# Kernel optimization log

Hardware: AMD Instinct MI355X
Metric: run time of the kernel (lower is better)

The kernel has to match this reference:

```python
import jax, jax.numpy as jnp
import numpy as np

B, N_L, N_T, H, NG, E, M = 8, 64, 512, 128, 10, 2048, 4096
BN_EPS = 1e-5


def _bn(x, g, b, m, v):
    # eval-mode BatchNorm1d
    return (x - m) * jax.lax.rsqrt(v + BN_EPS) * g + b


def _to_dense_batch(x, batch, n_batch, n_max):
    # batch is sorted; position within each graph = idx - first idx of that graph
    first = jnp.searchsorted(batch, jnp.arange(n_batch))
    pos = jnp.arange(x.shape[0]) - first[batch]
    dense = jnp.zeros((n_batch, n_max, x.shape[-1]), x.dtype).at[batch, pos].set(x)
    mask = jnp.zeros((n_batch, n_max), bool).at[batch, pos].set(True)
    return dense, mask


def setup_inputs() -> dict:
    key = jax.random.key(0)
    ks = jax.random.split(key, 32)
    rn = lambda k, s, sc=0.05: (jax.random.normal(k, s, jnp.float32) * sc)
    inp = {}
    inp["lig_s"] = rn(ks[0], (B * N_L, H), 1.0)
    inp["pro_s"] = rn(ks[1], (B * N_T, H), 1.0)
    inp["lig_batch"] = jnp.repeat(jnp.arange(B), N_L)
    inp["pro_batch"] = jnp.repeat(jnp.arange(B), N_T)
    inp["donar_idx"] = jax.random.randint(ks[2], (M,), 0, B * N_L * N_T, jnp.int32)
    inp["edge_index"] = jax.random.randint(ks[3], (2, E), 0, B * N_L, jnp.int32)
    # MLP head (Linear 2H->H + BN)
    inp["mlp_w"] = rn(ks[4], (2 * H, H)); inp["mlp_b"] = rn(ks[5], (H,))
    inp["mlp_g"] = 1.0 + rn(ks[6], (H,), 0.1); inp["mlp_be"] = rn(ks[7], (H,))
    inp["mlp_m"] = rn(ks[8], (H,)); inp["mlp_v"] = jax.random.uniform(ks[9], (H,), jnp.float32) + 0.5
    # start_donar_selector (Linear 2H->H + BN + Linear H->1 + sigmoid)
    inp["sel_w1"] = rn(ks[10], (2 * H, H)); inp["sel_b1"] = rn(ks[11], (H,))
    inp["sel_g"] = 1.0 + rn(ks[12], (H,), 0.1); inp["sel_be"] = rn(ks[13], (H,))
    inp["sel_m"] = rn(ks[14], (H,)); inp["sel_v"] = jax.random.uniform(ks[15], (H,), jnp.float32) + 0.5
    inp["sel_w2"] = rn(ks[16], (H, 1)); inp["sel_b2"] = rn(ks[17], (1,))
    # MDN heads
    inp["pi_w"] = rn(ks[18], (H, NG)); inp["pi_b"] = rn(ks[19], (NG,))
    inp["sg_w"] = rn(ks[20], (H, NG)); inp["sg_b"] = rn(ks[21], (NG,))
    inp["mu_w"] = rn(ks[22], (H, NG)); inp["mu_b"] = rn(ks[23], (NG,))
    # atom / bond type heads
    inp["at_w"] = rn(ks[24], (H, 18)); inp["at_b"] = rn(ks[25], (18,))
    inp["bt_w"] = rn(ks[26], (2 * H, 5)); inp["bt_b"] = rn(ks[27], (5,))
    return inp


def reference(lig_s, pro_s, lig_batch, pro_batch, donar_idx, edge_index,
              mlp_w, mlp_b, mlp_g, mlp_be, mlp_m, mlp_v,
              sel_w1, sel_b1, sel_g, sel_be, sel_m, sel_v, sel_w2, sel_b2,
              pi_w, pi_b, sg_w, sg_b, mu_w, mu_b, at_w, at_b, bt_w, bt_b):
    h_l, l_mask = _to_dense_batch(lig_s, lig_batch, B, N_L)   # (B,N_L,H)
    h_t, t_mask = _to_dense_batch(pro_s, pro_batch, B, N_T)   # (B,N_T,H)
    # dense pairwise broadcast + concat (masks are all-True by construction,
    # so C[C_mask] == flatten)
    pl = jnp.broadcast_to(h_l[:, :, None, :], (B, N_L, N_T, H))
    pt = jnp.broadcast_to(h_t[:, None, :, :], (B, N_L, N_T, H))
    Cpair = jnp.concatenate([pl, pt], -1).reshape(B * N_L * N_T, 2 * H)
    C_mask = l_mask[:, :, None] & t_mask[:, None, :]
    # donor-metal selector on gathered pairs
    dm = Cpair[donar_idx]
    sel_h = jax.nn.elu(_bn(dm @ sel_w1 + sel_b1, sel_g, sel_be, sel_m, sel_v))
    coordinated_donar = jax.nn.sigmoid(sel_h @ sel_w2 + sel_b2)[:, 0]
    # shared pair MLP (dropout is identity in eval)
    Ch = jax.nn.elu(_bn(Cpair @ mlp_w + mlp_b, mlp_g, mlp_be, mlp_m, mlp_v))
    pi = jax.nn.softmax(Ch @ pi_w + pi_b, -1)
    sigma = jax.nn.elu(Ch @ sg_w + sg_b) + 1.1
    mu = jax.nn.elu(Ch @ mu_w + mu_b) + 1.0
    C_batch = jnp.repeat(jnp.arange(B), N_L * N_T)
    atom_types = lig_s @ at_w + at_b
    bond_types = jnp.concatenate([lig_s[edge_index[0]], lig_s[edge_index[1]]], 1) @ bt_w + bt_b
    return (pi, sigma, mu, C_batch, atom_types, bond_types, coordinated_donar, C_mask)
```

## Files before the change

kernel.cpp:

```cpp
#include <hip/hip_runtime.h>

#define NL 64
#define NT 512
#define BB 8
#define HH 128
#define NE 2048
#define NM 4096

static constexpr size_t OUT_PI = 0;
static constexpr size_t OUT_SG = 2621440;
static constexpr size_t OUT_MU = 5242880;
static constexpr size_t OUT_CB = 7864320;
static constexpr size_t OUT_AT = 8126464;
static constexpr size_t OUT_BT = 8135680;
static constexpr size_t OUT_CD = 8145920;
static constexpr size_t OUT_CM = 8150016;

__device__ __forceinline__ float bf2f(ushort u) {
    union { uint i; float f; } v; v.i = ((uint)u) << 16; return v.f;
}
__device__ __forceinline__ float bflo(uint u) {
    union { uint i; float f; } v; v.i = u << 16; return v.f;
}
__device__ __forceinline__ float bfhi(uint u) {
    union { uint i; float f; } v; v.i = u & 0xffff0000u; return v.f;
}
__device__ __forceinline__ ushort f2bf(float f) {
    union { float f; uint u; } v; v.f = f;
    uint u = v.u + 0x7fffu + ((v.u >> 16) & 1u);
    return (ushort)(u >> 16);
}
__device__ __forceinline__ float eluf(float x) { return x > 0.f ? x : (__expf(x) - 1.f); }

__device__ __forceinline__ float ldv(const float* p, int i) { return p[i]; }
__device__ __forceinline__ float ldv(const ushort* p, int i) { return bf2f(p[i]); }

template <typename T>
__device__ void prep_w_body(const T* piw, const T* pib, const T* sgw, const T* sgb,
                            const T* muw, const T* mub, const T* selw2, const T* selb2,
                            float* Wp, float* biasv, float* sel2f) {
    int k = threadIdx.x;
#pragma unroll
    for (int g = 0; g < 10; ++g) {
        Wp[k * 32 + g]      = ldv(piw, k * 10 + g);
        Wp[k * 32 + 10 + g] = ldv(sgw, k * 10 + g);
        Wp[k * 32 + 20 + g] = ldv(muw, k * 10 + g);
    }
    Wp[k * 32 + 30] = 0.f; Wp[k * 32 + 31] = 0.f;
    sel2f[k] = ldv(selw2, k);
    if (k == 0) {
#pragma unroll
        for (int g = 0; g < 10; ++g) {
            biasv[g] = ldv(pib, g); biasv[10 + g] = ldv(sgb, g); biasv[20 + g] = ldv(mub, g);
        }
        biasv[30] = 0.f; biasv[31] = 0.f;
        sel2f[128] = ldv(selb2, 0);
    }
}
__global__ void kprep0(const uint* sniffsrc, const void* piw, const void* pib,
                       const void* sgw, const void* sgb, const void* muw, const void* mub,
                       const void* selw2, const void* selb2,
                       int* flag, float* Wp, float* biasv, float* sel2f) {
    __shared__ int sflag;
    if (threadIdx.x == 0) {
        int c = 0;
        for (int i = 0; i < 32; ++i) {
            uint lo = sniffsrc[i] & 0xFFFFu;
            if (lo >= 0x3F00u && lo <= 0x3FC0u) ++c;
        }
        sflag = (c >= 24) ? 0 : 1;
        *flag = sflag;
    }
    __syncthreads();
    if (sflag) prep_w_body((const float*)piw, (const float*)pib, (const float*)sgw, (const float*)sgb,
                           (const float*)muw, (const float*)mub, (const float*)selw2, (const float*)selb2,
                           Wp, biasv, sel2f);
    else       prep_w_body((const ushort*)piw, (const ushort*)pib, (const ushort*)sgw, (const ushort*)sgb,
                           (const ushort*)muw, (const ushort*)mub, (const ushort*)selw2, (const ushort*)selb2,
                           Wp, biasv, sel2f);
}

template <typename T>
__device__ void prep_lig_body(const T* lig, const T* mlpw, const T* selw1,
                              const T* mg, const T* mv, const T* sg_, const T* sv,
                              const T* atw, const T* atb,
                              float* Lp, float* SLp, float* out) {
    __shared__ float x[HH];
    int r = blockIdx.x, n = threadIdx.x;
    x[n] = ldv(lig, r * HH + n);
    __syncthreads();
    float accL = 0.f, accS = 0.f;
#pragma unroll 8
    for (int k = 0; k < HH; ++k) {
        float xv = x[k];
        accL = fmaf(xv, ldv(mlpw, k * HH + n), accL);
        accS = fmaf(xv, ldv(selw1, k * HH + n), accS);
    }
    float sM = ldv(mg, n) * rsqrtf(ldv(mv, n) + 1e-5f);
    float sS = ldv(sg_, n) * rsqrtf(ldv(sv, n) + 1e-5f);
    Lp[r * HH + n]  = accL * sM;
    SLp[r * HH + n] = accS * sS;
    if (n < 18) {
        float a = 0.f;
#pragma unroll 8
        for (int k = 0; k < HH; ++k) a = fmaf(x[k], ldv(atw, k * 18 + n), a);
        out[OUT_AT + r * 18 + n] = a + ldv(atb, n);
    }
}
__global__ void kprep_lig(const void* lig, const void* mlpw, const void* selw1,
                          const void* mg, const void* mv, const void* sg_, const void* sv,
                          const void* atw, const void* atb, const int* flag,
                          float* Lp, float* SLp, float* out) {
    if (*flag) prep_lig_body((const float*)lig, (const float*)mlpw, (const float*)selw1,
                             (const float*)mg, (const float*)mv, (const float*)sg_, (const float*)sv,
                             (const float*)atw, (const float*)atb, Lp, SLp, out);
    else       prep_lig_body((const ushort*)lig, (const ushort*)mlpw, (const ushort*)selw1,
                             (const ushort*)mg, (const ushort*)mv, (const ushort*)sg_, (const ushort*)sv,
                             (const ushort*)atw, (const ushort*)atb, Lp, SLp, out);
}

template <typename T>
__device__ void prep_pro_bond_body(const T* pro, const T* mlpw, const T* selw1,
                                   const T* mb, const T* mg, const T* mbe, const T* mm, const T* mv,
                                   const T* sb1, const T* sg_, const T* sbe, const T* sm, const T* sv,
                                   const T* lig, const int* edge, const T* btw, const T* btb,
                                   ushort* Tp, ushort* STp, float* out) {
    __shared__ float x[4][HH];
    int r0 = blockIdx.x * 4, n = threadIdx.x;
#pragma unroll
    for (int r = 0; r < 4; ++r) x[r][n] = ldv(pro, (r0 + r) * HH + n);
    __syncthreads();
    float aT0 = 0, aT1 = 0, aT2 = 0, aT3 = 0, aS0 = 0, aS1 = 0, aS2 = 0, aS3 = 0;
#pragma unroll 4
    for (int k = 0; k < HH; ++k) {
        float wM = ldv(mlpw, (HH + k) * HH + n);
        float wS = ldv(selw1, (HH + k) * HH + n);
        float x0 = x[0][k], x1 = x[1][k], x2 = x[2][k], x3 = x[3][k];
        aT0 = fmaf(x0, wM, aT0); aS0 = fmaf(x0, wS, aS0);
        aT1 = fmaf(x1, wM, aT1); aS1 = fmaf(x1, wS, aS1);
        aT2 = fmaf(x2, wM, aT2); aS2 = fmaf(x2, wS, aS2);
        aT3 = fmaf(x3, wM, aT3); aS3 = fmaf(x3, wS, aS3);
    }
    float sM = ldv(mg, n) * rsqrtf(ldv(mv, n) + 1e-5f);
    float sS = ldv(sg_, n) * rsqrtf(ldv(sv, n) + 1e-5f);
    float offM = ldv(mb, n) * sM + ldv(mbe, n) - ldv(mm, n) * sM;
    float offS = ldv(sb1, n) * sS + ldv(sbe, n) - ldv(sm, n) * sS;
    Tp[(r0 + 0) * HH + n] = f2bf(aT0 * sM + offM);  STp[(r0 + 0) * HH + n] = f2bf(aS0 * sS + offS);
    Tp[(r0 + 1) * HH + n] = f2bf(aT1 * sM + offM);  STp[(r0 + 1) * HH + n] = f2bf(aS1 * sS + offS);
    Tp[(r0 + 2) * HH + n] = f2bf(aT2 * sM + offM);  STp[(r0 + 2) * HH + n] = f2bf(aS2 * sS + offS);
    Tp[(r0 + 3) * HH + n] = f2bf(aT3 * sM + offM);  STp[(r0 + 3) * HH + n] = f2bf(aS3 * sS + offS);

    int widx = n >> 6, lane = n & 63;
    int e = blockIdx.x * 2 + widx;
    int e0 = edge[e], e1 = edge[NE + e];
    int k0 = lane * 2;
    float a0 = ldv(lig, e0 * HH + k0), a1 = ldv(lig, e0 * HH + k0 + 1);
    float b0 = ldv(lig, e1 * HH + k0), b1 = ldv(lig, e1 * HH + k0 + 1);
    float acc[5];
#pragma unroll
    for (int c = 0; c < 5; ++c) {
        acc[c] = a0 * ldv(btw, k0 * 5 + c) + a1 * ldv(btw, (k0 + 1) * 5 + c)
               + b0 * ldv(btw, (HH + k0) * 5 + c) + b1 * ldv(btw, (HH + k0 + 1) * 5 + c);
    }
#pragma unroll
    for (int c = 0; c < 5; ++c)
        for (int off = 32; off > 0; off >>= 1) acc[c] += __shfl_xor(acc[c], off, 64);
    if (lane == 0) {
#pragma unroll
        for (int c = 0; c < 5; ++c) out[OUT_BT + e * 5 + c] = acc[c] + ldv(btb, c);
    }
}
__global__ void kprep_pro_bond(const void* pro, const void* mlpw, const void* selw1,
                               const void* mb, const void* mg, const void* mbe, const void* mm, const void* mv,
                               const void* sb1, const void* sg_, const void* sbe, const void* sm, const void* sv,
                               const void* lig, const int* edge, const void* btw, const void* btb,
                               const int* flag, ushort* Tp, ushort* STp, float* out) {
    if (*flag) prep_pro_bond_body((const float*)pro, (const float*)mlpw, (const float*)selw1,
                                  (const float*)mb, (const float*)mg, (const float*)mbe, (const float*)mm, (const float*)mv,
                                  (const float*)sb1, (const float*)sg_, (const float*)sbe, (const float*)sm, (const float*)sv,
                                  (const float*)lig, edge, (const float*)btw, (const float*)btb, Tp, STp, out);
    else       prep_pro_bond_body((const ushort*)pro, (const ushort*)mlpw, (const ushort*)selw1,
                                  (const ushort*)mb, (const ushort*)mg, (const ushort*)mbe, (const ushort*)mm, (const ushort*)mv,
                                  (const ushort*)sb1, (const ushort*)sg_, (const ushort*)sbe, (const ushort*)sm, (const ushort*)sv,
                                  (const ushort*)lig, edge, (const ushort*)btw, (const ushort*)btb, Tp, STp, out);
}

__global__ __launch_bounds__(256, 4) void kmain(const ushort* __restrict__ Tp, const float* __restrict__ Lp,
                                                const float* __restrict__ Wp, const float* __restrict__ biasv,
                                                const float* __restrict__ SLp, const ushort* __restrict__ STp,
                                                const int* __restrict__ donar, const float* __restrict__ sel2f,
                                                float* __restrict__ out) {
    __shared__ uint  ldsTu[64 * 65];
    __shared__ float ldsL[4 * 132];
    int bid = blockIdx.x;
    int jt = bid & 7, it = (bid >> 3) & 15, b = bid >> 7;
    int j0 = jt * 64, i0 = it * 4;
    int tid = threadIdx.x;

    const uint* srcT = (const uint*)(Tp + (size_t)(b * NT + j0) * HH);
#pragma unroll
    for (int q = 0; q < 4; ++q) {
        int t = tid + q * 256;
        uint4 v = ((const uint4*)srcT)[t];
        int j = t >> 4, c0 = (t & 15) * 4;
        uint* dst = &ldsTu[j * 65 + c0];
        dst[0] = v.x; dst[1] = v.y; dst[2] = v.z; dst[3] = v.w;
    }
    if (tid < 128) {
        int r = tid >> 5, c = (tid & 31) * 4;
        float4 v = *(const float4*)(Lp + (size_t)(b * NL + i0 + r) * HH + c);
        *(float4*)&ldsL[r * 132 + c] = v;
    }
    __syncthreads();

    int lane_j = tid & 63, widx = tid >> 6;
    const uint*  trowp = &ldsTu[lane_j * 65];
    const float* lsrow = &ldsL[widx * 132];
    float acc[30];
#pragma unroll
    for (int g = 0; g < 30; ++g) acc[g] = 0.f;
#pragma unroll 8
    for (int m = 0; m < 64; ++m) {
        uint tp2 = trowp[m];
        float ch0 = eluf(lsrow[2 * m]     + bflo(tp2));
        float ch1 = eluf(lsrow[2 * m + 1] + bfhi(tp2));
        const float* w0 = Wp + (2 * m) * 32;
        const float* w1 = Wp + (2 * m + 1) * 32;
#pragma unroll
        for (int g = 0; g < 30; ++g)
            acc[g] = fmaf(ch1, w1[g], fmaf(ch0, w0[g], acc[g]));
    }

    int li = b * NL + i0 + widx;
    size_t p = (size_t)li * NT + j0 + lane_j;
    float v0[10], ex[10];
    float mx = -1e30f;
#pragma unroll
    for (int g = 0; g < 10; ++g) { v0[g] = acc[g] + biasv[g]; mx = fmaxf(mx, v0[g]); }
    float s = 0.f;
#pragma unroll
    for (int g = 0; g < 10; ++g) { ex[g] = __expf(v0[g] - mx); s += ex[g]; }
    float inv = 1.f / s;
    float2* opi = (float2*)(out + OUT_PI + p * 10);
#pragma unroll
    for (int gg = 0; gg < 5; ++gg) opi[gg] = make_float2(ex[2 * gg] * inv, ex[2 * gg + 1] * inv);
    float2* osg = (float2*)(out + OUT_SG + p * 10);
#pragma unroll
    for (int gg = 0; gg < 5; ++gg) {
        osg[gg] = make_float2(eluf(acc[10 + 2 * gg] + biasv[10 + 2 * gg]) + 1.1f,
                              eluf(acc[11 + 2 * gg] + biasv[11 + 2 * gg]) + 1.1f);
    }
    float2* omu = (float2*)(out + OUT_MU + p * 10);
#pragma unroll
    for (int gg = 0; gg < 5; ++gg) {
        omu[gg] = make_float2(eluf(acc[20 + 2 * gg] + biasv[20 + 2 * gg]) + 1.0f,
                              eluf(acc[21 + 2 * gg] + biasv[21 + 2 * gg]) + 1.0f);
    }
    out[OUT_CB + p] = (float)b;
    out[OUT_CM + p] = 1.0f;

    int w = bid * 4 + widx;
    int d = donar[w];
    int dli = d >> 9;
    int dtj = ((d >> 15) << 9) + (d & 511);
    int k0 = lane_j << 1;
    float2 sl = *(const float2*)(SLp + (size_t)dli * HH + k0);
    uint stp = ((const uint*)STp)[dtj * 64 + lane_j];
    float x0 = eluf(sl.x + bflo(stp));
    float x1 = eluf(sl.y + bfhi(stp));
    float ssum = x0 * sel2f[k0] + x1 * sel2f[k0 + 1];
    for (int off = 32; off > 0; off >>= 1) ssum += __shfl_xor(ssum, off, 64);
    if (lane_j == 0) {
        float z = ssum + sel2f[128];
        out[OUT_CD + w] = 1.f / (1.f + __expf(-z));
    }
}

extern "C" void kernel_launch(void* const* d_in, const int* in_sizes, int n_in,
                              void* d_out, int out_size, void* d_ws, size_t ws_size,
                              hipStream_t stream) {
    (void)in_sizes; (void)n_in; (void)out_size; (void)ws_size;
    float* out = (float*)d_out;

    char* wsb = (char*)d_ws;
    float*  Lp    = (float*)(wsb);
    float*  SLp   = (float*)(wsb + 262144);
    float*  Wp    = (float*)(wsb + 524288);
    float*  biasv = (float*)(wsb + 540672);
    float*  sel2f = (float*)(wsb + 540800);
    int*    flag  = (int*)  (wsb + 541328);
    ushort* Tp    = (ushort*)(wsb + 541344);
    ushort* STp   = (ushort*)(wsb + 1589920);

    kprep0<<<1, 128, 0, stream>>>((const uint*)d_in[11], d_in[20], d_in[21], d_in[22], d_in[23],
                                  d_in[24], d_in[25], d_in[18], d_in[19], flag, Wp, biasv, sel2f);
    kprep_lig<<<512, 128, 0, stream>>>(d_in[0], d_in[6], d_in[12], d_in[8], d_in[11],
                                       d_in[14], d_in[17], d_in[26], d_in[27], flag, Lp, SLp, out);
    kprep_pro_bond<<<1024, 128, 0, stream>>>(d_in[1], d_in[6], d_in[12],
                                             d_in[7], d_in[8], d_in[9], d_in[10], d_in[11],
                                             d_in[13], d_in[14], d_in[15], d_in[16], d_in[17],
                                             d_in[0], (const int*)d_in[5], d_in[28], d_in[29],
                                             flag, Tp, STp, out);
    kmain<<<1024, 256, 0, stream>>>(Tp, Lp, Wp, biasv, SLp, STp, (const int*)d_in[4], sel2f, out);
}
```

Before: 193.0 us.

## Use bf16 MFMA for pair-head projection and merge prep kernels into one launch

The main kernel now does the 128x30 head projection with 16x16x32 bf16 MFMA instructions instead of scalar FMAs. Activations are ELU'd and packed to bf16 in registers, weights are prepacked into MFMA fragment layout, and results are transposed through LDS for the epilogue. The three prep kernels and the dtype-sniffing flag are merged into one launch, with each block re-sniffing the dtype itself. This cuts launch overhead and ALU work, but adds bf16 rounding of activations and weights and a larger LDS footprint that may reduce occupancy.

```diff
diff --git a/kernel.cpp b/kernel.cpp
--- a/kernel.cpp
+++ b/kernel.cpp
@@ -16,6 +16,9 @@
 static constexpr size_t OUT_CD = 8145920;
 static constexpr size_t OUT_CM = 8150016;
 
+typedef __attribute__((ext_vector_type(8))) short bf16x8;
+typedef __attribute__((ext_vector_type(4))) float f32x4;
+
 __device__ __forceinline__ float bf2f(ushort u) {
     union { uint i; float f; } v; v.i = ((uint)u) << 16; return v.f;
 }
@@ -31,62 +34,22 @@
     return (ushort)(u >> 16);
 }
 __device__ __forceinline__ float eluf(float x) { return x > 0.f ? x : (__expf(x) - 1.f); }
+__device__ __forceinline__ uint pkelu2(float a, float b) {
+    a = eluf(a); b = eluf(b);
+    union { float f; uint u; } ua, ub; ua.f = a; ub.f = b;
+    return ((ua.u + 0x8000u) >> 16) | ((ub.u + 0x8000u) & 0xffff0000u);
+}
 
 __device__ __forceinline__ float ldv(const float* p, int i) { return p[i]; }
 __device__ __forceinline__ float ldv(const ushort* p, int i) { return bf2f(p[i]); }
 
 template <typename T>
-__device__ void prep_w_body(const T* piw, const T* pib, const T* sgw, const T* sgb,
-                            const T* muw, const T* mub, const T* selw2, const T* selb2,
-                            float* Wp, float* biasv, float* sel2f) {
-    int k = threadIdx.x;
-#pragma unroll
-    for (int g = 0; g < 10; ++g) {
-        Wp[k * 32 + g]      = ldv(piw, k * 10 + g);
-        Wp[k * 32 + 10 + g] = ldv(sgw, k * 10 + g);
-        Wp[k * 32 + 20 + g] = ldv(muw, k * 10 + g);
-    }
-    Wp[k * 32 + 30] = 0.f; Wp[k * 32 + 31] = 0.f;
-    sel2f[k] = ldv(selw2, k);
-    if (k == 0) {
-#pragma unroll
-        for (int g = 0; g < 10; ++g) {
-            biasv[g] = ldv(pib, g); biasv[10 + g] = ldv(sgb, g); biasv[20 + g] = ldv(mub, g);
-        }
-        biasv[30] = 0.f; biasv[31] = 0.f;
-        sel2f[128] = ldv(selb2, 0);
-    }
-}
-__global__ void kprep0(const uint* sniffsrc, const void* piw, const void* pib,
-                       const void* sgw, const void* sgb, const void* muw, const void* mub,
-                       const void* selw2, const void* selb2,
-                       int* flag, float* Wp, float* biasv, float* sel2f) {
-    __shared__ int sflag;
-    if (threadIdx.x == 0) {
-        int c = 0;
-        for (int i = 0; i < 32; ++i) {
-            uint lo = sniffsrc[i] & 0xFFFFu;
-            if (lo >= 0x3F00u && lo <= 0x3FC0u) ++c;
-        }
-        sflag = (c >= 24) ? 0 : 1;
-        *flag = sflag;
-    }
-    __syncthreads();
-    if (sflag) prep_w_body((const float*)piw, (const float*)pib, (const float*)sgw, (const float*)sgb,
-                           (const float*)muw, (const float*)mub, (const float*)selw2, (const float*)selb2,
-                           Wp, biasv, sel2f);
-    else       prep_w_body((const ushort*)piw, (const ushort*)pib, (const ushort*)sgw, (const ushort*)sgb,
-                           (const ushort*)muw, (const ushort*)mub, (const ushort*)selw2, (const ushort*)selb2,
-                           Wp, biasv, sel2f);
-}
-
-template <typename T>
-__device__ void prep_lig_body(const T* lig, const T* mlpw, const T* selw1,
+__device__ void prep_lig_part(int r, const T* lig, const T* mlpw, const T* selw1,
                               const T* mg, const T* mv, const T* sg_, const T* sv,
                               const T* atw, const T* atb,
                               float* Lp, float* SLp, float* out) {
     __shared__ float x[HH];
-    int r = blockIdx.x, n = threadIdx.x;
+    int n = threadIdx.x;
     x[n] = ldv(lig, r * HH + n);
     __syncthreads();
     float accL = 0.f, accS = 0.f;
@@ -107,26 +70,15 @@
         out[OUT_AT + r * 18 + n] = a + ldv(atb, n);
     }
 }
-__global__ void kprep_lig(const void* lig, const void* mlpw, const void* selw1,
-                          const void* mg, const void* mv, const void* sg_, const void* sv,
-                          const void* atw, const void* atb, const int* flag,
-                          float* Lp, float* SLp, float* out) {
-    if (*flag) prep_lig_body((const float*)lig, (const float*)mlpw, (const float*)selw1,
-                             (const float*)mg, (const float*)mv, (const float*)sg_, (const float*)sv,
-                             (const float*)atw, (const float*)atb, Lp, SLp, out);
-    else       prep_lig_body((const ushort*)lig, (const ushort*)mlpw, (const ushort*)selw1,
-                             (const ushort*)mg, (const ushort*)mv, (const ushort*)sg_, (const ushort*)sv,
-                             (const ushort*)atw, (const ushort*)atb, Lp, SLp, out);
-}
 
 template <typename T>
-__device__ void prep_pro_bond_body(const T* pro, const T* mlpw, const T* selw1,
+__device__ void prep_pro_bond_part(int pb, const T* pro, const T* mlpw, const T* selw1,
                                    const T* mb, const T* mg, const T* mbe, const T* mm, const T* mv,
                                    const T* sb1, const T* sg_, const T* sbe, const T* sm, const T* sv,
                                    const T* lig, const int* edge, const T* btw, const T* btb,
                                    ushort* Tp, ushort* STp, float* out) {
     __shared__ float x[4][HH];
-    int r0 = blockIdx.x * 4, n = threadIdx.x;
+    int r0 = pb * 4, n = threadIdx.x;
 #pragma unroll
     for (int r = 0; r < 4; ++r) x[r][n] = ldv(pro, (r0 + r) * HH + n);
     __syncthreads();
@@ -151,7 +103,7 @@
     Tp[(r0 + 3) * HH + n] = f2bf(aT3 * sM + offM);  STp[(r0 + 3) * HH + n] = f2bf(aS3 * sS + offS);
 
     int widx = n >> 6, lane = n & 63;
-    int e = blockIdx.x * 2 + widx;
+    int e = pb * 2 + widx;
     int e0 = edge[e], e1 = edge[NE + e];
     int k0 = lane * 2;
     float a0 = ldv(lig, e0 * HH + k0), a1 = ldv(lig, e0 * HH + k0 + 1);
@@ -170,91 +122,181 @@
         for (int c = 0; c < 5; ++c) out[OUT_BT + e * 5 + c] = acc[c] + ldv(btb, c);
     }
 }
-__global__ void kprep_pro_bond(const void* pro, const void* mlpw, const void* selw1,
-                               const void* mb, const void* mg, const void* mbe, const void* mm, const void* mv,
-                               const void* sb1, const void* sg_, const void* sbe, const void* sm, const void* sv,
-                               const void* lig, const int* edge, const void* btw, const void* btb,
-                               const int* flag, ushort* Tp, ushort* STp, float* out) {
-    if (*flag) prep_pro_bond_body((const float*)pro, (const float*)mlpw, (const float*)selw1,
-                                  (const float*)mb, (const float*)mg, (const float*)mbe, (const float*)mm, (const float*)mv,
-                                  (const float*)sb1, (const float*)sg_, (const float*)sbe, (const float*)sm, (const float*)sv,
-                                  (const float*)lig, edge, (const float*)btw, (const float*)btb, Tp, STp, out);
-    else       prep_pro_bond_body((const ushort*)pro, (const ushort*)mlpw, (const ushort*)selw1,
-                                  (const ushort*)mb, (const ushort*)mg, (const ushort*)mbe, (const ushort*)mm, (const ushort*)mv,
-                                  (const ushort*)sb1, (const ushort*)sg_, (const ushort*)sbe, (const ushort*)sm, (const ushort*)sv,
-                                  (const ushort*)lig, edge, (const ushort*)btw, (const ushort*)btb, Tp, STp, out);
-}
-
-__global__ __launch_bounds__(256, 4) void kmain(const ushort* __restrict__ Tp, const float* __restrict__ Lp,
-                                                const float* __restrict__ Wp, const float* __restrict__ biasv,
-                                                const float* __restrict__ SLp, const ushort* __restrict__ STp,
-                                                const int* __restrict__ donar, const float* __restrict__ sel2f,
-                                                float* __restrict__ out) {
-    __shared__ uint  ldsTu[64 * 65];
-    __shared__ float ldsL[4 * 132];
+
+template <typename T>
+__device__ void prep_w_part(const T* piw, const T* pib, const T* sgw, const T* sgb,
+                            const T* muw, const T* mub, const T* selw2, const T* selb2,
+                            uint4* Wb, float* biasv, float* sel2f) {
+    int t = threadIdx.x;
+    for (int f = t; f < 768; f += 128) {
+        int tile = f >> 8, ks = (f >> 6) & 3, ln = f & 63;
+        int n = ln & 15, q = ln >> 4;
+        const T* Wh = (tile == 0) ? piw : ((tile == 1) ? sgw : muw);
+        uint pr[4];
+#pragma unroll
+        for (int tt = 0; tt < 4; ++tt) {
+            int k = ks * 32 + q * 8 + 2 * tt;
+            ushort lo = (n < 10) ? f2bf(ldv(Wh, k * 10 + n)) : (ushort)0;
+            ushort hi = (n < 10) ? f2bf(ldv(Wh, (k + 1) * 10 + n)) : (ushort)0;
+            pr[tt] = (uint)lo | ((uint)hi << 16);
+        }
+        uint4 u; u.x = pr[0]; u.y = pr[1]; u.z = pr[2]; u.w = pr[3];
+        Wb[f] = u;
+    }
+    sel2f[t] = ldv(selw2, t);
+    if (t == 0) {
+#pragma unroll
+        for (int g = 0; g < 10; ++g) {
+            biasv[g] = ldv(pib, g); biasv[10 + g] = ldv(sgb, g); biasv[20 + g] = ldv(mub, g);
+        }
+        biasv[30] = 0.f; biasv[31] = 0.f;
+        sel2f[128] = ldv(selb2, 0);
+    }
+}
+
+template <typename T>
+__device__ void prep_all_body(int bid,
+    const T* lig, const T* pro, const T* mlpw, const T* selw1,
+    const T* mb, const T* mg, const T* mbe, const T* mm, const T* mv,
+    const T* sb1, const T* sg_, const T* sbe, const T* sm, const T* sv,
+    const T* atw, const T* atb, const T* btw, const T* btb,
+    const T* piw, const T* pib, const T* sgw, const T* sgb, const T* muw, const T* mub,
+    const T* selw2, const T* selb2, const int* edge,
+    float* Lp, float* SLp, ushort* Tp, ushort* STp, uint4* Wb, float* biasv, float* sel2f,
+    float* out) {
+    if (bid < 512) {
+        prep_lig_part(bid, lig, mlpw, selw1, mg, mv, sg_, sv, atw, atb, Lp, SLp, out);
+    } else if (bid < 1536) {
+        prep_pro_bond_part(bid - 512, pro, mlpw, selw1, mb, mg, mbe, mm, mv,
+                           sb1, sg_, sbe, sm, sv, lig, edge, btw, btb, Tp, STp, out);
+    } else {
+        prep_w_part(piw, pib, sgw, sgb, muw, mub, selw2, selb2, Wb, biasv, sel2f);
+    }
+}
+
+__global__ void kprep_all(
+    const void* lig, const void* pro, const void* mlpw, const void* selw1,
+    const void* mb, const void* mg, const void* mbe, const void* mm, const void* mv,
+    const void* sb1, const void* sg_, const void* sbe, const void* sm, const void* sv,
+    const void* atw, const void* atb, const void* btw, const void* btb,
+    const void* piw, const void* pib, const void* sgw, const void* sgb, const void* muw, const void* mub,
+    const void* selw2, const void* selb2, const int* edge,
+    float* Lp, float* SLp, ushort* Tp, ushort* STp, uint4* Wb, float* biasv, float* sel2f,
+    float* out) {
+    const uint* w = (const uint*)mv;
+    int c = 0;
+#pragma unroll
+    for (int i = 0; i < 32; ++i) { uint lo = w[i] & 0xFFFFu; c += (lo >= 0x3F00u && lo <= 0x3FC0u); }
     int bid = blockIdx.x;
+    if (c < 24) {
+        prep_all_body(bid, (const float*)lig, (const float*)pro, (const float*)mlpw, (const float*)selw1,
+                      (const float*)mb, (const float*)mg, (const float*)mbe, (const float*)mm, (const float*)mv,
+                      (const float*)sb1, (const float*)sg_, (const float*)sbe, (const float*)sm, (const float*)sv,
+                      (const float*)atw, (const float*)atb, (const float*)btw, (const float*)btb,
+                      (const float*)piw, (const float*)pib, (const float*)sgw, (const float*)sgb,
+                      (const float*)muw, (const float*)mub, (const float*)selw2, (const float*)selb2,
+                      edge, Lp, SLp, Tp, STp, Wb, biasv, sel2f, out);
+    } else {
+        prep_all_body(bid, (const ushort*)lig, (const ushort*)pro, (const ushort*)mlpw, (const ushort*)selw1,
+                      (const ushort*)mb, (const ushort*)mg, (const ushort*)mbe, (const ushort*)mm, (const ushort*)mv,
+                      (const ushort*)sb1, (const ushort*)sg_, (const ushort*)sbe, (const ushort*)sm, (const ushort*)sv,
+                      (const ushort*)atw, (const ushort*)atb, (const ushort*)btw, (const ushort*)btb,
+                      (const ushort*)piw, (const ushort*)pib, (const ushort*)sgw, (const ushort*)sgb,
+                      (const ushort*)muw, (const ushort*)mub, (const ushort*)selw2, (const ushort*)selb2,
+                      edge, Lp, SLp, Tp, STp, Wb, biasv, sel2f, out);
+    }
+}
+
+__global__ __launch_bounds__(256) void kmain(
+    const ushort* __restrict__ Tp, const float* __restrict__ Lp, const uint4* __restrict__ Wb,
+    const float* __restrict__ biasv, const float* __restrict__ SLp, const ushort* __restrict__ STp,
+    const int* __restrict__ donar, const float* __restrict__ sel2f, float* __restrict__ out) {
+    __shared__ float ep[4 * 64 * 33];
+    int bid = blockIdx.x, tid = threadIdx.x;
     int jt = bid & 7, it = (bid >> 3) & 15, b = bid >> 7;
     int j0 = jt * 64, i0 = it * 4;
-    int tid = threadIdx.x;
-
-    const uint* srcT = (const uint*)(Tp + (size_t)(b * NT + j0) * HH);
-#pragma unroll
-    for (int q = 0; q < 4; ++q) {
-        int t = tid + q * 256;
-        uint4 v = ((const uint4*)srcT)[t];
-        int j = t >> 4, c0 = (t & 15) * 4;
-        uint* dst = &ldsTu[j * 65 + c0];
-        dst[0] = v.x; dst[1] = v.y; dst[2] = v.z; dst[3] = v.w;
-    }
-    if (tid < 128) {
-        int r = tid >> 5, c = (tid & 31) * 4;
-        float4 v = *(const float4*)(Lp + (size_t)(b * NL + i0 + r) * HH + c);
-        *(float4*)&ldsL[r * 132 + c] = v;
-    }
-    __syncthreads();
-
-    int lane_j = tid & 63, widx = tid >> 6;
-    const uint*  trowp = &ldsTu[lane_j * 65];
-    const float* lsrow = &ldsL[widx * 132];
-    float acc[30];
-#pragma unroll
-    for (int g = 0; g < 30; ++g) acc[g] = 0.f;
-#pragma unroll 8
-    for (int m = 0; m < 64; ++m) {
-        uint tp2 = trowp[m];
-        float ch0 = eluf(lsrow[2 * m]     + bflo(tp2));
-        float ch1 = eluf(lsrow[2 * m + 1] + bfhi(tp2));
-        const float* w0 = Wp + (2 * m) * 32;
-        const float* w1 = Wp + (2 * m + 1) * 32;
-#pragma unroll
-        for (int g = 0; g < 30; ++g)
-            acc[g] = fmaf(ch1, w1[g], fmaf(ch0, w0[g], acc[g]));
-    }
+    int lane = tid & 63, widx = tid >> 6;
+    int m16 = lane & 15, quad = lane >> 4;
+
+    const float* Lg = Lp + (size_t)(b * NL + i0 + widx) * HH + quad * 8;
+    f32x4 Lr[4][2];
+#pragma unroll
+    for (int ks = 0; ks < 4; ++ks) {
+        Lr[ks][0] = *(const f32x4*)(Lg + ks * 32);
+        Lr[ks][1] = *(const f32x4*)(Lg + ks * 32 + 4);
+    }
+
+    const ushort* Tbase = Tp + (size_t)(b * NT + j0) * HH;
+    f32x4 acc[4][3];
+#pragma unroll
+    for (int mt = 0; mt < 4; ++mt)
+#pragma unroll
+        for (int t = 0; t < 3; ++t) acc[mt][t] = (f32x4){0.f, 0.f, 0.f, 0.f};
+
+#pragma unroll
+    for (int ks = 0; ks < 4; ++ks) {
+        bf16x8 Bfr[3];
+#pragma unroll
+        for (int t = 0; t < 3; ++t) {
+            uint4 wv = Wb[(t * 4 + ks) * 64 + lane];
+            Bfr[t] = *(bf16x8*)&wv;
+        }
+        float l0 = Lr[ks][0][0], l1 = Lr[ks][0][1], l2 = Lr[ks][0][2], l3 = Lr[ks][0][3];
+        float l4 = Lr[ks][1][0], l5 = Lr[ks][1][1], l6 = Lr[ks][1][2], l7 = Lr[ks][1][3];
+#pragma unroll
+        for (int mt = 0; mt < 4; ++mt) {
+            uint4 tv = *(const uint4*)(Tbase + (size_t)(mt * 16 + m16) * HH + ks * 32 + quad * 8);
+            uint4 af;
+            af.x = pkelu2(l0 + bflo(tv.x), l1 + bfhi(tv.x));
+            af.y = pkelu2(l2 + bflo(tv.y), l3 + bfhi(tv.y));
+            af.z = pkelu2(l4 + bflo(tv.z), l5 + bfhi(tv.z));
+            af.w = pkelu2(l6 + bflo(tv.w), l7 + bfhi(tv.w));
+            bf16x8 A = *(bf16x8*)&af;
+            acc[mt][0] = __builtin_amdgcn_mfma_f32_16x16x32_bf16(A, Bfr[0], acc[mt][0], 0, 0, 0);
+            acc[mt][1] = __builtin_amdgcn_mfma_f32_16x16x32_bf16(A, Bfr[1], acc[mt][1], 0, 0, 0);
+            acc[mt][2] = __builtin_amdgcn_mfma_f32_16x16x32_bf16(A, Bfr[2], acc[mt][2], 0, 0, 0);
+        }
+    }
+
+    float* myep = ep + widx * 2112;
+    if (m16 < 10) {
+#pragma unroll
+        for (int mt = 0; mt < 4; ++mt)
+#pragma unroll
+            for (int t = 0; t < 3; ++t)
+#pragma unroll
+                for (int r = 0; r < 4; ++r)
+                    myep[(mt * 16 + quad * 4 + r) * 33 + t * 10 + m16] = acc[mt][t][r];
+    }
+    float a2[30];
+    const float* arow = myep + lane * 33;
+#pragma unroll
+    for (int g = 0; g < 30; ++g) a2[g] = arow[g];
 
     int li = b * NL + i0 + widx;
-    size_t p = (size_t)li * NT + j0 + lane_j;
-    float v0[10], ex[10];
+    size_t p = (size_t)li * NT + j0 + lane;
+    float v0[10], exv[10];
     float mx = -1e30f;
 #pragma unroll
-    for (int g = 0; g < 10; ++g) { v0[g] = acc[g] + biasv[g]; mx = fmaxf(mx, v0[g]); }
+    for (int g = 0; g < 10; ++g) { v0[g] = a2[g] + biasv[g]; mx = fmaxf(mx, v0[g]); }
     float s = 0.f;
 #pragma unroll
-    for (int g = 0; g < 10; ++g) { ex[g] = __expf(v0[g] - mx); s += ex[g]; }
+    for (int g = 0; g < 10; ++g) { exv[g] = __expf(v0[g] - mx); s += exv[g]; }
     float inv = 1.f / s;
     float2* opi = (float2*)(out + OUT_PI + p * 10);
 #pragma unroll
-    for (int gg = 0; gg < 5; ++gg) opi[gg] = make_float2(ex[2 * gg] * inv, ex[2 * gg + 1] * inv);
+    for (int gg = 0; gg < 5; ++gg) opi[gg] = make_float2(exv[2 * gg] * inv, exv[2 * gg + 1] * inv);
     float2* osg = (float2*)(out + OUT_SG + p * 10);
 #pragma unroll
     for (int gg = 0; gg < 5; ++gg) {
-        osg[gg] = make_float2(eluf(acc[10 + 2 * gg] + biasv[10 + 2 * gg]) + 1.1f,
-                              eluf(acc[11 + 2 * gg] + biasv[11 + 2 * gg]) + 1.1f);
+        osg[gg] = make_float2(eluf(a2[10 + 2 * gg] + biasv[10 + 2 * gg]) + 1.1f,
+                              eluf(a2[11 + 2 * gg] + biasv[11 + 2 * gg]) + 1.1f);
     }
     float2* omu = (float2*)(out + OUT_MU + p * 10);
 #pragma unroll
     for (int gg = 0; gg < 5; ++gg) {
-        omu[gg] = make_float2(eluf(acc[20 + 2 * gg] + biasv[20 + 2 * gg]) + 1.0f,
-                              eluf(acc[21 + 2 * gg] + biasv[21 + 2 * gg]) + 1.0f);
+        omu[gg] = make_float2(eluf(a2[20 + 2 * gg] + biasv[20 + 2 * gg]) + 1.0f,
+                              eluf(a2[21 + 2 * gg] + biasv[21 + 2 * gg]) + 1.0f);
     }
     out[OUT_CB + p] = (float)b;
     out[OUT_CM + p] = 1.0f;
@@ -263,14 +305,14 @@
     int d = donar[w];
     int dli = d >> 9;
     int dtj = ((d >> 15) << 9) + (d & 511);
-    int k0 = lane_j << 1;
+    int k0 = lane << 1;
     float2 sl = *(const float2*)(SLp + (size_t)dli * HH + k0);
-    uint stp = ((const uint*)STp)[dtj * 64 + lane_j];
+    uint stp = ((const uint*)STp)[dtj * 64 + lane];
     float x0 = eluf(sl.x + bflo(stp));
     float x1 = eluf(sl.y + bfhi(stp));
     float ssum = x0 * sel2f[k0] + x1 * sel2f[k0 + 1];
     for (int off = 32; off > 0; off >>= 1) ssum += __shfl_xor(ssum, off, 64);
-    if (lane_j == 0) {
+    if (lane == 0) {
         float z = ssum + sel2f[128];
         out[OUT_CD + w] = 1.f / (1.f + __expf(-z));
     }
@@ -285,21 +327,19 @@
     char* wsb = (char*)d_ws;
     float*  Lp    = (float*)(wsb);
     float*  SLp   = (float*)(wsb + 262144);
-    float*  Wp    = (float*)(wsb + 524288);
-    float*  biasv = (float*)(wsb + 540672);
-    float*  sel2f = (float*)(wsb + 540800);
-    int*    flag  = (int*)  (wsb + 541328);
-    ushort* Tp    = (ushort*)(wsb + 541344);
-    ushort* STp   = (ushort*)(wsb + 1589920);
-
-    kprep0<<<1, 128, 0, stream>>>((const uint*)d_in[11], d_in[20], d_in[21], d_in[22], d_in[23],
-                                  d_in[24], d_in[25], d_in[18], d_in[19], flag, Wp, biasv, sel2f);
-    kprep_lig<<<512, 128, 0, stream>>>(d_in[0], d_in[6], d_in[12], d_in[8], d_in[11],
-                                       d_in[14], d_in[17], d_in[26], d_in[27], flag, Lp, SLp, out);
-    kprep_pro_bond<<<1024, 128, 0, stream>>>(d_in[1], d_in[6], d_in[12],
-                                             d_in[7], d_in[8], d_in[9], d_in[10], d_in[11],
-                                             d_in[13], d_in[14], d_in[15], d_in[16], d_in[17],
-                                             d_in[0], (const int*)d_in[5], d_in[28], d_in[29],
-                                             flag, Tp, STp, out);
-    kmain<<<1024, 256, 0, stream>>>(Tp, Lp, Wp, biasv, SLp, STp, (const int*)d_in[4], sel2f, out);
-}
+    uint4*  Wb    = (uint4*)(wsb + 524288);
+    float*  biasv = (float*)(wsb + 536576);
+    float*  sel2f = (float*)(wsb + 536704);
+    ushort* Tp    = (ushort*)(wsb + 537248);
+    ushort* STp   = (ushort*)(wsb + 1585824);
+
+    kprep_all<<<1537, 128, 0, stream>>>(
+        d_in[0], d_in[1], d_in[6], d_in[12],
+        d_in[7], d_in[8], d_in[9], d_in[10], d_in[11],
+        d_in[13], d_in[14], d_in[15], d_in[16], d_in[17],
+        d_in[26], d_in[27], d_in[28], d_in[29],
+        d_in[20], d_in[21], d_in[22], d_in[23], d_in[24], d_in[25],
+        d_in[18], d_in[19], (const int*)d_in[5],
+        Lp, SLp, Tp, STp, Wb, biasv, sel2f, out);
+    kmain<<<1024, 256, 0, stream>>>(Tp, Lp, Wb, biasv, SLp, STp, (const int*)d_in[4], sel2f, out);
+}
```

Measured after the change: 161.5 us. -16.4%, faster.
